# Performance work log

Hardware: AMD Instinct MI355X
Metric: run time of the kernel (lower is better)

The kernel has to match this reference:

```python
import jax, jax.numpy as jnp
import numpy as np

B, T, D_IN, H, N_CLS = 64, 1024, 64, 256, 32


def _gru_dir(x, Wih, Whh, bih, bhh):
    # x: [B,T,Din]; Wih: [3H,Din]; Whh: [3H,H]. Runs FORWARD in time (the
    # original feeds the bidirectional GRU one step at a time, so the
    # 'backward' direction also advances forward in time).
    h0 = jnp.zeros((x.shape[0], Whh.shape[-1]), dtype=x.dtype)
    xg = jnp.einsum('btd,gd->btg', x, Wih) + bih  # [B,T,3H] precomputed input gates
    xg = jnp.swapaxes(xg, 0, 1)                   # [T,B,3H]
    Hh = Whh.shape[-1]

    def step(h, xt):
        gh = h @ Whh.T + bhh
        r = jax.nn.sigmoid(xt[:, :Hh] + gh[:, :Hh])
        z = jax.nn.sigmoid(xt[:, Hh:2 * Hh] + gh[:, Hh:2 * Hh])
        n = jnp.tanh(xt[:, 2 * Hh:] + r * gh[:, 2 * Hh:])
        h = (1.0 - z) * n + z * h
        return h, h

    _, ys = jax.lax.scan(step, h0, xg)  # ys: [T,B,H]
    return jnp.swapaxes(ys, 0, 1)       # [B,T,H]


def _encoder(x, Wih0, Whh0, bih0, bhh0, Wih12, Whh12, bih12, bhh12):
    # layer 0: input dim D_IN; layers 1-2: input dim 2H
    y = x
    for layer in range(3):
        if layer == 0:
            Wi, Wh, bi, bh = Wih0, Whh0, bih0, bhh0
        else:
            Wi, Wh, bi, bh = (Wih12[layer - 1], Whh12[layer - 1],
                              bih12[layer - 1], bhh12[layer - 1])
        out0 = _gru_dir(y, Wi[0], Wh[0], bi[0], bh[0])
        out1 = _gru_dir(y, Wi[1], Wh[1], bi[1], bh[1])
        y = jnp.concatenate([out0, out1], axis=-1)  # [B,T,2H]
    return y


def setup_inputs() -> dict:
    key = jax.random.key(0)
    ks = jax.random.split(key, 12)
    s = 0.05
    inp = {
        'input_tensor': jax.random.normal(ks[0], (B, T, D_IN), jnp.float32),
        'seq_len': jax.random.randint(ks[1], (B,), 1, T + 1, jnp.int32),
        'Wih0': jax.random.normal(ks[2], (2, 3 * H, D_IN), jnp.float32) * s,
        'Whh0': jax.random.normal(ks[3], (2, 3 * H, H), jnp.float32) * s,
        'bih0': jax.random.normal(ks[4], (2, 3 * H), jnp.float32) * s,
        'bhh0': jax.random.normal(ks[5], (2, 3 * H), jnp.float32) * s,
        'Wih12': jax.random.normal(ks[6], (2, 2, 3 * H, 2 * H), jnp.float32) * s,
        'Whh12': jax.random.normal(ks[7], (2, 2, 3 * H, H), jnp.float32) * s,
        'bih12': jax.random.normal(ks[8], (2, 2, 3 * H), jnp.float32) * s,
        'bhh12': jax.random.normal(ks[9], (2, 2, 3 * H), jnp.float32) * s,
        'Wc': jax.random.normal(ks[10], (N_CLS, 2 * H), jnp.float32) * s,
        'bc': jax.random.normal(ks[11], (N_CLS,), jnp.float32) * s,
    }
    return inp


def reference(input_tensor, seq_len, Wih0, Whh0, bih0, bhh0,
              Wih12, Whh12, bih12, bhh12, Wc, bc):
    enc = _encoder(input_tensor, Wih0, Whh0, bih0, bhh0,
                   Wih12, Whh12, bih12, bhh12)          # [B,T,2H]
    idx = seq_len - 1
    hidden = enc[jnp.arange(enc.shape[0]), idx, :]       # [B,2H] final state per length
    pred = hidden @ Wc.T + bc                            # single Linear, no ReLU (1 layer)
    return pred
```

## Files before the change

kernel.cpp:

```cpp
#include <hip/hip_runtime.h>
#include <hip/hip_bf16.h>
#include <hip/hip_fp16.h>

typedef unsigned int u32;
typedef unsigned short u16;
typedef __attribute__((ext_vector_type(4))) float f32x4;
typedef __attribute__((ext_vector_type(8))) _Float16 h16x8;
typedef __attribute__((ext_vector_type(4))) u32 u32x4;

#define NL2E  (-1.4426950408889634f)
#define P2L2E ( 2.8853900817779268f)

__device__ __forceinline__ u16 f2h(float f) {
  _Float16 h = (_Float16)f;
  return __builtin_bit_cast(u16, h);
}
__device__ __forceinline__ float h2f(u16 u) {
  return (float)__builtin_bit_cast(_Float16, u);
}
__device__ __forceinline__ void gload16(const void* g, void* l) {
  __builtin_amdgcn_global_load_lds((const __attribute__((address_space(1))) u32*)g,
                                   (__attribute__((address_space(3))) u32*)l, 16, 0, 0);
}

#define BARRIER() do {                                      \
    __builtin_amdgcn_sched_barrier(0);                      \
    asm volatile("s_waitcnt lgkmcnt(0)" ::: "memory");      \
    __builtin_amdgcn_sched_barrier(0);                      \
    __builtin_amdgcn_s_barrier();                           \
    __builtin_amdgcn_sched_barrier(0);                      \
  } while (0)

__global__ void convh_k(const float* __restrict__ s, u16* __restrict__ d, int n4) {
  int i = blockIdx.x * 256 + threadIdx.x;
  if (i < n4) {
    float4 f = ((const float4*)s)[i];
    ushort4 u;
    u.x = f2h(f.x); u.y = f2h(f.y); u.z = f2h(f.z); u.w = f2h(f.w);
    ((ushort4*)d)[i] = u;
  }
}

__global__ void convpair_k(const float* __restrict__ s, u16* __restrict__ dh,
                           u16* __restrict__ dl, int n4) {
  int i = blockIdx.x * 256 + threadIdx.x;
  if (i < n4) {
    float4 f = ((const float4*)s)[i];
    ushort4 uh, ul;
    uh.x = f2h(f.x); ul.x = f2h(f.x - h2f(uh.x));
    uh.y = f2h(f.y); ul.y = f2h(f.y - h2f(uh.y));
    uh.z = f2h(f.z); ul.z = f2h(f.z - h2f(uh.z));
    uh.w = f2h(f.w); ul.w = f2h(f.w - h2f(uh.w));
    ((ushort4*)dh)[i] = uh;
    ((ushort4*)dl)[i] = ul;
  }
}

__global__ void badd_k(const float* __restrict__ bih0, const float* __restrict__ bhh0,
                       const float* __restrict__ bih12, const float* __restrict__ bhh12,
                       float* __restrict__ badd) {
  int i = blockIdx.x * 256 + threadIdx.x;
  if (i < 4608) {
    int lay = i / 1536, r = i % 1536;
    int dd = r / 768, gg = r % 768;
    float bi = lay == 0 ? bih0[dd * 768 + gg] : bih12[((lay - 1) * 2 + dd) * 768 + gg];
    float bh = lay == 0 ? bhh0[dd * 768 + gg] : bhh12[((lay - 1) * 2 + dd) * 768 + gg];
    badd[i] = bi + (gg < 512 ? bh : 0.f);
  }
}

template<int K, int PAIR>
__global__ __launch_bounds__(256, 2) void gemm_k(
    const u16* __restrict__ A, const u16* __restrict__ Bh,
    const u16* __restrict__ Bl, const float* __restrict__ badd_l,
    float* __restrict__ xg, int t0)
{
  __shared__ __attribute__((aligned(16))) char sm[49152];
  const int tid = threadIdx.x;
  const int w = tid >> 6, l = tid & 63;
  const int g = l >> 4, lm = l & 15;
  const int wr = w >> 1, wc = w & 1;

  int bx = blockIdx.x;
  int wg = (bx & 7) * 48 + (bx >> 3);
  int nb = wg % 12, mb = wg / 12;

  u32 offA[4], offB[4];
#pragma unroll
  for (int c = 0; c < 4; ++c) {
    int x = c * 4096 + tid * 16;
    int row = x >> 7;
    int blog = (x - row * 16) & 127;
    offA[c] = (u32)((nb * 128 + row) * (K * 2) + blog);
    int m = mb * 128 + row;
    int b2 = m & 63, tl2 = m >> 6;
    if constexpr (K == 64) offB[c] = (u32)((b2 * 1024 + t0 + tl2) * 128 + blog);
    else                   offB[c] = (u32)((b2 * 64 + tl2) * 1024 + blog);
  }
  u32 aoff[4][2], boff[4][2];
#pragma unroll
  for (int i = 0; i < 4; ++i) {
    int rowA = wr * 64 + i * 16 + lm;
    int rowB = wc * 64 + i * 16 + lm;
#pragma unroll
    for (int kk = 0; kk < 2; ++kk) {
      aoff[i][kk] = rowA * 128 + ((g * 16 + kk * 64 + rowA * 16) & 127);
      boff[i][kk] = rowB * 128 + ((g * 16 + kk * 64 + rowB * 16) & 127);
    }
  }

  f32x4 acc[4][4];
#pragma unroll
  for (int a = 0; a < 4; ++a)
#pragma unroll
    for (int c = 0; c < 4; ++c) acc[a][c] = (f32x4){0.f, 0.f, 0.f, 0.f};

  const char* Ac = (const char*)A;
  const char* Bhc = (const char*)Bh;
  const char* Blc = (const char*)Bl;

#pragma unroll 1
  for (int ki = 0; ki < K / 64; ++ki) {
    __syncthreads();
#pragma unroll
    for (int c = 0; c < 4; ++c) {
      gload16(Ac + offA[c], sm + c * 4096 + w * 1024);
      gload16(Bhc + offB[c], sm + 16384 + c * 4096 + w * 1024);
      if constexpr (PAIR) gload16(Blc + offB[c], sm + 32768 + c * 4096 + w * 1024);
      offA[c] += 128; offB[c] += 128;
    }
    __syncthreads();
#pragma unroll
    for (int kk = 0; kk < 2; ++kk) {
      h16x8 af[4], bh4[4];
#pragma unroll
      for (int a = 0; a < 4; ++a) af[a] = *(const h16x8*)(sm + aoff[a][kk]);
#pragma unroll
      for (int c = 0; c < 4; ++c) bh4[c] = *(const h16x8*)(sm + 16384 + boff[c][kk]);
#pragma unroll
      for (int a = 0; a < 4; ++a)
#pragma unroll
        for (int c = 0; c < 4; ++c)
          acc[a][c] = __builtin_amdgcn_mfma_f32_16x16x32_f16(af[a], bh4[c], acc[a][c], 0, 0, 0);
      if constexpr (PAIR) {
        h16x8 bl4[4];
#pragma unroll
        for (int c = 0; c < 4; ++c) bl4[c] = *(const h16x8*)(sm + 32768 + boff[c][kk]);
#pragma unroll
        for (int a = 0; a < 4; ++a)
#pragma unroll
          for (int c = 0; c < 4; ++c)
            acc[a][c] = __builtin_amdgcn_mfma_f32_16x16x32_f16(af[a], bl4[c], acc[a][c], 0, 0, 0);
      }
    }
  }

  float4 bd[4];
#pragma unroll
  for (int a = 0; a < 4; ++a)
    bd[a] = *(const float4*)(badd_l + nb * 128 + (wr * 4 + a) * 16 + 4 * g);

#pragma unroll
  for (int a = 0; a < 4; ++a) {
    int n_t = nb * 8 + wr * 4 + a;
    int dir = n_t >= 48 ? 1 : 0;
    int nw = (n_t - 48 * dir) * 16 + g * 4;
    int q = nw >> 8, kb = nw & 255;
    int w_r = kb >> 5, hf = (kb >> 4) & 1, g_r = (kb >> 2) & 3;
    int biw = lm & 7;
    int tid_r = w_r * 64 + g_r * 16 + hf * 8 + biw;
#pragma unroll
    for (int c = 0; c < 4; ++c) {
      int m_t = mb * 8 + wc * 4 + c;
      int tl = m_t >> 2;
      int bg8w = (m_t & 3) * 2 + (lm >> 3);
      size_t blk = (size_t)((dir * 64 + tl) * 8 + bg8w);
      float4 v = make_float4(acc[a][c][0] + bd[a].x, acc[a][c][1] + bd[a].y,
                             acc[a][c][2] + bd[a].z, acc[a][c][3] + bd[a].w);
      *(float4*)(xg + blk * 6144 + q * 2048 + tid_r * 4) = v;
    }
  }
}

__global__ __launch_bounds__(512, 2) void recur3_k(
    const float* __restrict__ xg0, const float* __restrict__ xg1,
    const float* __restrict__ xg2, const u16* __restrict__ whhb,
    const float* __restrict__ bhh0, const float* __restrict__ bhh12,
    u16* __restrict__ yA, u16* __restrict__ yB, u16* __restrict__ y16,
    float* __restrict__ Gws, float* __restrict__ hsws, int s)
{
  __shared__ __attribute__((aligned(16))) char sm[65536];
  const int bx = blockIdx.x;
  const int L = bx >> 4;
  const int c = s - L;
  if (c < 0 || c > 15) return;
  const int t0 = c * 64;
  const float* xg = L == 0 ? xg0 : (L == 1 ? xg1 : xg2);
  const u16* whh = whhb + (size_t)L * 393216;
  const float* bhh = L == 0 ? bhh0 : (L == 1 ? bhh12 : bhh12 + 1536);
  u16* y; int ybs;
  if (L == 0)      { y = yA;  ybs = 64 * 512; }
  else if (L == 1) { y = yB;  ybs = 64 * 512; }
  else             { y = y16 + (size_t)t0 * 512; ybs = 1024 * 512; }
  float* Gst = Gws + (size_t)L * (16 * 512 * 24);
  float* hst = hsws + (size_t)L * (16 * 512 * 4);

  const int sub = bx & 15;
  const int d = sub & 1, bg8 = sub >> 1;
  const int tid = threadIdx.x;
  const int w = tid >> 6, l = tid & 63;
  const int g = l >> 4, lm = l & 15;
  const int bi = lm & 7, half = lm >> 3;

  const u16* wp = whh + (size_t)d * 196608;

  h16x8 bfr[2][3][7];
#pragma unroll
  for (int jj = 0; jj < 2; ++jj)
#pragma unroll
    for (int q = 0; q < 3; ++q)
#pragma unroll
      for (int kk = 0; kk < 7; ++kk)
        bfr[jj][q][kk] = *(const h16x8*)(wp + (size_t)(q * 256 + (2 * w + jj) * 16 + lm) * 256
                                         + kk * 32 + g * 8);
#pragma unroll
  for (int i = 0; i < 6; ++i) {
    int v = i * 512 + tid;
    int row = v >> 2, g2 = v & 3;
    *(u32x4*)(sm + 16384 + g2 * 12288 + row * 16) =
        *(const u32x4*)((const char*)wp + row * 512 + 448 + g2 * 16);
  }
  {
    u32x4 z4 = {0u, 0u, 0u, 0u};
    *(u32x4*)(sm + 4096 + (tid >> 8) * 8192 + (tid & 255) * 16) = z4;
  }

  const int k0f0 = 32 * w + 4 * g;
  const int k0f1 = 32 * w + 16 + 4 * g;
  const int k0t = 32 * w + 16 * half + 4 * g;

  f32x4 G[2][3];
  f32x4 hs;
  if (t0 == 0) {
    G[0][0] = (f32x4){0.f, 0.f, 0.f, 0.f};
    G[0][1] = (f32x4){0.f, 0.f, 0.f, 0.f};
    G[1][0] = (f32x4){0.f, 0.f, 0.f, 0.f};
    G[1][1] = (f32x4){0.f, 0.f, 0.f, 0.f};
    G[0][2] = *(const f32x4*)(bhh + d * 768 + 512 + k0f0);
    G[1][2] = *(const f32x4*)(bhh + d * 768 + 512 + k0f1);
    hs = (f32x4){0.f, 0.f, 0.f, 0.f};
  } else {
    const f32x4* gsrc = (const f32x4*)(Gst + (size_t)(sub * 512 + tid) * 24);
#pragma unroll
    for (int jj = 0; jj < 2; ++jj) {
      G[jj][0] = gsrc[jj * 3]; G[jj][1] = gsrc[jj * 3 + 1]; G[jj][2] = gsrc[jj * 3 + 2];
    }
    hs = *(const f32x4*)(hst + (size_t)(sub * 512 + tid) * 4);
  }

  const int dwr = bi * 512 + ((k0t * 2) ^ (bi << 4));
  int drd[8];
#pragma unroll
  for (int kk = 0; kk < 8; ++kk) drd[kk] = lm * 512 + ((kk * 64 + g * 16) ^ (lm << 4));
  const int a7 = 16384 + g * 12288 + (2 * w) * 256 + lm * 16;

  const char* xsrc = (const char*)xg + (size_t)(d * 512 + bg8) * 24576 + tid * 16;
  const char* xnx = xsrc + 196608;
  const int batch = bg8 * 8 + bi;
  u16* yb = y + (size_t)batch * ybs + d * 256;

  f32x4 xs[3];
  xs[0] = *(const f32x4*)(xsrc);
  xs[1] = *(const f32x4*)(xsrc + 8192);
  xs[2] = *(const f32x4*)(xsrc + 16384);

#define STEP(P, PRE, VMSTR) do {                                                       \
    asm volatile("s_waitcnt " VMSTR ::: "memory");                                     \
    __builtin_amdgcn_sched_barrier(0);                                                 \
    f32x4 sz0, sz1, sz2;                                                               \
    _Pragma("unroll")                                                                  \
    for (int e = 0; e < 4; ++e) {                                                      \
      sz0[e] = __shfl_xor(G[1][0][e], 8);                                              \
      sz1[e] = __shfl_xor(G[1][1][e], 8);                                              \
      sz2[e] = __shfl_xor(G[1][2][e], 8);                                              \
    }                                                                                  \
    f32x4 Gr = half ? sz0 : G[0][0];                                                   \
    f32x4 Gz = half ? sz1 : G[0][1];                                                   \
    f32x4 Gn = half ? sz2 : G[0][2];                                                   \
    float dd[4];                                                                       \
    _Pragma("unroll")                                                                  \
    for (int e = 0; e < 4; ++e) {                                                      \
      float pr = Gr[e] + xs[0][e];                                                     \
      float pz = Gz[e] + xs[1][e];                                                     \
      float r = __builtin_amdgcn_rcpf(1.f + __builtin_amdgcn_exp2f(pr * NL2E));        \
      float z = __builtin_amdgcn_rcpf(1.f + __builtin_amdgcn_exp2f(pz * NL2E));        \
      float np = xs[2][e] + r * Gn[e];                                                 \
      float nt = 1.f - 2.f * __builtin_amdgcn_rcpf(1.f + __builtin_amdgcn_exp2f(np * P2L2E)); \
      float h = nt + z * (hs[e] - nt);                                                 \
      dd[e] = h - hs[e];                                                               \
    }                                                                                  \
    u32 pk0 = __builtin_bit_cast(u32, __builtin_amdgcn_cvt_pkrtz(dd[0], dd[1]));       \
    u32 pk1 = __builtin_bit_cast(u32, __builtin_amdgcn_cvt_pkrtz(dd[2], dd[3]));       \
    hs[0] += h2f((u16)(pk0 & 0xffffu)); hs[1] += h2f((u16)(pk0 >> 16));                \
    hs[2] += h2f((u16)(pk1 & 0xffffu)); hs[3] += h2f((u16)(pk1 >> 16));                \
    uint2 hv = make_uint2((u32)f2h(hs[0]) | ((u32)f2h(hs[1]) << 16),                   \
                          (u32)f2h(hs[2]) | ((u32)f2h(hs[3]) << 16));                  \
    *(uint2*)(sm + (P) * 8192 + dwr) = make_uint2(pk0, pk1);                           \
    if (PRE) {                                                                         \
      xs[0] = *(const f32x4*)(xnx);                                                    \
      xs[1] = *(const f32x4*)(xnx + 8192);                                             \
      xs[2] = *(const f32x4*)(xnx + 16384);                                            \
      xnx += 196608;                                                                   \
    }                                                                                  \
    __builtin_amdgcn_sched_barrier(0);              \
    *(uint2*)(yb + k0t) = hv;                                                          \
    yb += 512;                                                                         \
    BARRIER();                                      \
    __builtin_amdgcn_s_setprio(1);                                                     \
    {                                                                                  \
      h16x8 cur[8];                                                                    \
      _Pragma("unroll")                                                                \
      for (int kk = 0; kk < 8; ++kk)                                                   \
        cur[kk] = *(const h16x8*)(sm + (P) * 8192 + drd[kk]);                          \
      _Pragma("unroll")                                                                \
      for (int kk = 0; kk < 7; ++kk)                                                   \
        _Pragma("unroll")                                                              \
        for (int jj = 0; jj < 2; ++jj) {                                               \
          G[jj][0] = __builtin_amdgcn_mfma_f32_16x16x32_f16(bfr[jj][0][kk], cur[kk], G[jj][0], 0, 0, 0); \
          G[jj][1] = __builtin_amdgcn_mfma_f32_16x16x32_f16(bfr[jj][1][kk], cur[kk], G[jj][1], 0, 0, 0); \
          G[jj][2] = __builtin_amdgcn_mfma_f32_16x16x32_f16(bfr[jj][2][kk], cur[kk], G[jj][2], 0, 0, 0); \
        }                                                                              \
      _Pragma("unroll")                                                                \
      for (int q = 0; q < 3; ++q)                                                      \
        _Pragma("unroll")                                                              \
        for (int jj = 0; jj < 2; ++jj) {                                               \
          h16x8 af = *(const h16x8*)(sm + a7 + q * 4096 + jj * 256);                   \
          G[jj][q] = __builtin_amdgcn_mfma_f32_16x16x32_f16(af, cur[7], G[jj][q], 0, 0, 0); \
        }                                                                              \
    }                                                                                  \
    __builtin_amdgcn_s_setprio(0);                                                     \
  } while (0)

  STEP(0, 1, "vmcnt(0)");
#pragma unroll 1
  for (int t2 = 0; t2 < 31; ++t2) {
    STEP(1, 1, "vmcnt(1)");
    STEP(0, 1, "vmcnt(1)");
  }
  STEP(1, 0, "vmcnt(1)");
#undef STEP

  f32x4* gdst = (f32x4*)(Gst + (size_t)(sub * 512 + tid) * 24);
#pragma unroll
  for (int jj = 0; jj < 2; ++jj) {
    gdst[jj * 3] = G[jj][0]; gdst[jj * 3 + 1] = G[jj][1]; gdst[jj * 3 + 2] = G[jj][2];
  }
  *(f32x4*)(hst + (size_t)(sub * 512 + tid) * 4) = hs;
}

__global__ void cls_k(const u16* __restrict__ y2, const int* __restrict__ sl,
                      const float* __restrict__ Wc, const float* __restrict__ bc,
                      float* __restrict__ out) {
  int b = blockIdx.x * 8 + (threadIdx.x >> 5);
  int cc = threadIdx.x & 31;
  int t = sl[b] - 1; t = t < 0 ? 0 : (t > 1023 ? 1023 : t);
  const u16* hr = y2 + (size_t)(b * 1024 + t) * 512;
  float s = 0.f;
  for (int k = 0; k < 512; k += 4) {
    ushort4 hv = *(const ushort4*)(hr + k);
    float4 wv = *(const float4*)(Wc + cc * 512 + k);
    s += h2f(hv.x) * wv.x + h2f(hv.y) * wv.y + h2f(hv.z) * wv.z + h2f(hv.w) * wv.w;
  }
  out[b * 32 + cc] = s + bc[cc];
}

extern "C" void kernel_launch(void* const* d_in, const int* in_sizes, int n_in,
                              void* d_out, int out_size, void* d_ws, size_t ws_size,
                              hipStream_t stream)
{
  const float* x     = (const float*)d_in[0];
  const int*   sl    = (const int*)d_in[1];
  const float* Wih0  = (const float*)d_in[2];
  const float* Whh0  = (const float*)d_in[3];
  const float* bih0  = (const float*)d_in[4];
  const float* bhh0  = (const float*)d_in[5];
  const float* Wih12 = (const float*)d_in[6];
  const float* Whh12 = (const float*)d_in[7];
  const float* bih12 = (const float*)d_in[8];
  const float* bhh12 = (const float*)d_in[9];
  const float* Wc    = (const float*)d_in[10];
  const float* bc    = (const float*)d_in[11];
  float* out = (float*)d_out;

  char* ws = (char*)d_ws;
  float* xg0   = (float*)(ws);
  float* xg1   = (float*)(ws + 25165824);
  float* xg2   = (float*)(ws + 50331648);
  u16* yA      = (u16*)(ws + 75497472);
  u16* yB      = (u16*)(ws + 79691776);
  u16* y16     = (u16*)(ws + 83886080);
  u16* xhi     = (u16*)(ws + 150994944);
  u16* xlo     = (u16*)(ws + 159383552);
  u16* wih0h   = (u16*)(ws + 167772160);
  u16* wih12h  = (u16*)(ws + 167968768);
  u16* whhh    = (u16*)(ws + 171114496);
  float* badd  = (float*)(ws + 173473792);
  float* Gws   = (float*)(ws + 173492224);
  float* hsws  = (float*)(ws + 175851520);

  convpair_k<<<4096, 256, 0, stream>>>(x, xhi, xlo, 1048576);
  convh_k<<<96,   256, 0, stream>>>(Wih0, wih0h, 24576);
  convh_k<<<1536, 256, 0, stream>>>(Wih12, wih12h, 393216);
  convh_k<<<384,  256, 0, stream>>>(Whh0, whhh, 98304);
  convh_k<<<768,  256, 0, stream>>>(Whh12, whhh + 393216, 196608);
  badd_k<<<18,    256, 0, stream>>>(bih0, bhh0, bih12, bhh12, badd);

  for (int s = 0; s < 18; ++s) {
    if (s <= 15)
      gemm_k<64, 1><<<384, 256, 0, stream>>>(wih0h, xhi, xlo, badd, xg0, s * 64);
    if (s >= 1 && s <= 16)
      gemm_k<512, 0><<<384, 256, 0, stream>>>(wih12h, yA, yA, badd + 1536, xg1, 0);
    if (s >= 2)
      gemm_k<512, 0><<<384, 256, 0, stream>>>(wih12h + 786432, yB, yB, badd + 3072, xg2, 0);
    recur3_k<<<48, 512, 0, stream>>>(xg0, xg1, xg2, whhh, bhh0, bhh12,
                                     yA, yB, y16, Gws, hsws, s);
  }
  cls_k<<<8, 256, 0, stream>>>(y16, sl, Wc, bc, out);
}
```

Baseline: 2.315 ms.

## Merge per-layer input-gate GEMMs into one launch and duplicate h writes in recurrence

The three per-layer input-projection GEMM launches in each wavefront step are merged into one kernel with 1152 blocks, where the block index picks the layer and inactive layers exit early. This cuts launch count and lets the three GEMMs run at the same time. In the recurrent kernel, the cross-half shuffle of gate accumulators is replaced by a plain select. Each thread also writes its packed h delta to a second LDS row (bi+8), and the zero-fill of the upper rows is removed. This trades shuffles for an extra LDS store per step, but the G[1] select semantics change, so correctness depends on a matching MFMA layout not shown here.

```diff
diff --git a/kernel.cpp b/kernel.cpp
--- a/kernel.cpp
+++ b/kernel.cpp
@@ -70,18 +70,17 @@
 }
 
 template<int K, int PAIR>
-__global__ __launch_bounds__(256, 2) void gemm_k(
+__device__ __forceinline__ void gemm_body(
+    char* sm, int bx,
     const u16* __restrict__ A, const u16* __restrict__ Bh,
     const u16* __restrict__ Bl, const float* __restrict__ badd_l,
     float* __restrict__ xg, int t0)
 {
-  __shared__ __attribute__((aligned(16))) char sm[49152];
   const int tid = threadIdx.x;
   const int w = tid >> 6, l = tid & 63;
   const int g = l >> 4, lm = l & 15;
   const int wr = w >> 1, wc = w & 1;
 
-  int bx = blockIdx.x;
   int wg = (bx & 7) * 48 + (bx >> 3);
   int nb = wg % 12, mb = wg / 12;
 
@@ -179,6 +178,25 @@
                              acc[a][c][2] + bd[a].z, acc[a][c][3] + bd[a].w);
       *(float4*)(xg + blk * 6144 + q * 2048 + tid_r * 4) = v;
     }
+  }
+}
+
+__global__ __launch_bounds__(256, 2) void gemm3_k(
+    const u16* __restrict__ wih0h, const u16* __restrict__ xhi,
+    const u16* __restrict__ xlo, const u16* __restrict__ wih12h,
+    const u16* __restrict__ yA, const u16* __restrict__ yB,
+    const float* __restrict__ badd, float* __restrict__ xg0,
+    float* __restrict__ xg1, float* __restrict__ xg2, int s)
+{
+  __shared__ __attribute__((aligned(16))) char sm[49152];
+  int L = blockIdx.x / 384;
+  int bx = blockIdx.x - L * 384;
+  if (L == 0) {
+    if (s <= 15) gemm_body<64, 1>(sm, bx, wih0h, xhi, xlo, badd, xg0, s * 64);
+  } else if (L == 1) {
+    if (s >= 1 && s <= 16) gemm_body<512, 0>(sm, bx, wih12h, yA, yA, badd + 1536, xg1, 0);
+  } else {
+    if (s >= 2) gemm_body<512, 0>(sm, bx, wih12h + 786432, yB, yB, badd + 3072, xg2, 0);
   }
 }
 
@@ -230,10 +248,6 @@
     *(u32x4*)(sm + 16384 + g2 * 12288 + row * 16) =
         *(const u32x4*)((const char*)wp + row * 512 + 448 + g2 * 16);
   }
-  {
-    u32x4 z4 = {0u, 0u, 0u, 0u};
-    *(u32x4*)(sm + 4096 + (tid >> 8) * 8192 + (tid & 255) * 16) = z4;
-  }
 
   const int k0f0 = 32 * w + 4 * g;
   const int k0f1 = 32 * w + 16 + 4 * g;
@@ -258,7 +272,8 @@
     hs = *(const f32x4*)(hst + (size_t)(sub * 512 + tid) * 4);
   }
 
-  const int dwr = bi * 512 + ((k0t * 2) ^ (bi << 4));
+  const int dwr0 = bi * 512 + ((k0t * 2) ^ (bi << 4));
+  const int dwr1 = (bi + 8) * 512 + ((k0t * 2) ^ ((bi + 8) << 4));
   int drd[8];
 #pragma unroll
   for (int kk = 0; kk < 8; ++kk) drd[kk] = lm * 512 + ((kk * 64 + g * 16) ^ (lm << 4));
@@ -277,16 +292,13 @@
 #define STEP(P, PRE, VMSTR) do {                                                       \
     asm volatile("s_waitcnt " VMSTR ::: "memory");                                     \
     __builtin_amdgcn_sched_barrier(0);                                                 \
-    f32x4 sz0, sz1, sz2;                                                               \
+    f32x4 Gr, Gz, Gn;                                                                  \
     _Pragma("unroll")                                                                  \
     for (int e = 0; e < 4; ++e) {                                                      \
-      sz0[e] = __shfl_xor(G[1][0][e], 8);                                              \
-      sz1[e] = __shfl_xor(G[1][1][e], 8);                                              \
-      sz2[e] = __shfl_xor(G[1][2][e], 8);                                              \
+      Gr[e] = half ? G[1][0][e] : G[0][0][e];                                          \
+      Gz[e] = half ? G[1][1][e] : G[0][1][e];                                          \
+      Gn[e] = half ? G[1][2][e] : G[0][2][e];                                          \
     }                                                                                  \
-    f32x4 Gr = half ? sz0 : G[0][0];                                                   \
-    f32x4 Gz = half ? sz1 : G[0][1];                                                   \
-    f32x4 Gn = half ? sz2 : G[0][2];                                                   \
     float dd[4];                                                                       \
     _Pragma("unroll")                                                                  \
     for (int e = 0; e < 4; ++e) {                                                      \
@@ -305,7 +317,8 @@
     hs[2] += h2f((u16)(pk1 & 0xffffu)); hs[3] += h2f((u16)(pk1 >> 16));                \
     uint2 hv = make_uint2((u32)f2h(hs[0]) | ((u32)f2h(hs[1]) << 16),                   \
                           (u32)f2h(hs[2]) | ((u32)f2h(hs[3]) << 16));                  \
-    *(uint2*)(sm + (P) * 8192 + dwr) = make_uint2(pk0, pk1);                           \
+    *(uint2*)(sm + (P) * 8192 + dwr0) = make_uint2(pk0, pk1);                          \
+    *(uint2*)(sm + (P) * 8192 + dwr1) = make_uint2(pk0, pk1);                          \
     if (PRE) {                                                                         \
       xs[0] = *(const f32x4*)(xnx);                                                    \
       xs[1] = *(const f32x4*)(xnx + 8192);                                             \
@@ -416,12 +429,8 @@
   badd_k<<<18,    256, 0, stream>>>(bih0, bhh0, bih12, bhh12, badd);
 
   for (int s = 0; s < 18; ++s) {
-    if (s <= 15)
-      gemm_k<64, 1><<<384, 256, 0, stream>>>(wih0h, xhi, xlo, badd, xg0, s * 64);
-    if (s >= 1 && s <= 16)
-      gemm_k<512, 0><<<384, 256, 0, stream>>>(wih12h, yA, yA, badd + 1536, xg1, 0);
-    if (s >= 2)
-      gemm_k<512, 0><<<384, 256, 0, stream>>>(wih12h + 786432, yB, yB, badd + 3072, xg2, 0);
+    gemm3_k<<<1152, 256, 0, stream>>>(wih0h, xhi, xlo, wih12h, yA, yB,
+                                      badd, xg0, xg1, xg2, s);
     recur3_k<<<48, 512, 0, stream>>>(xg0, xg1, xg2, whhh, bhh0, bhh12,
                                      yA, yB, y16, Gws, hsws, s);
   }
```

After: 1.995 ms. 13.8% less time.
